# Performance work log

Hardware: AMD Instinct MI355X
Metric: run time of the kernel (lower is better)

The kernel has to match this reference:

```python
import jax, jax.numpy as jnp
import numpy as np

NH = 4
ATT = 16
COL = 64
AIS = 64
B = 8192
SK = 200


def setup_inputs() -> dict:
    key = jax.random.key(0)
    k1, k2, k3, k4, k5 = jax.random.split(key, 5)
    # Xavier-uniform bounds for [fan_in, fan_out] matrices
    def xavier(k, fan_in, fan_out):
        bound = float(np.sqrt(6.0 / (fan_in + fan_out)))
        return jax.random.uniform(k, (fan_in, fan_out), jnp.float32, -bound, bound)
    return {
        "query_input": jax.random.normal(k1, (B, 1, COL), jnp.float32),
        "action_list_input": jax.random.normal(k2, (B, SK, AIS), jnp.float32),
        "Q": xavier(k3, COL, ATT * NH),
        "K": xavier(k4, AIS, ATT * NH),
        "V": xavier(k5, AIS, ATT * NH),
    }


def reference(query_input, action_list_input, Q, K, V):
    b = query_input.shape[0]
    sq = query_input.shape[1]          # == 1 (required by final reshape)
    sk = action_list_input.shape[1]
    # projections
    q = jnp.tensordot(query_input, Q, axes=([-1], [0]))        # [B,Sq,NH*ATT]
    k = jnp.tensordot(action_list_input, K, axes=([-1], [0]))  # [B,Sk,NH*ATT]
    v = jnp.tensordot(action_list_input, V, axes=([-1], [0]))  # [B,Sk,NH*ATT]
    # split heads: chunk along last dim then stack on new leading dim -> [NH,B,S,ATT]
    qh = jnp.transpose(q.reshape(b, sq, NH, ATT), (2, 0, 1, 3))
    kh = jnp.transpose(k.reshape(b, sk, NH, ATT), (2, 0, 1, 3))
    vh = jnp.transpose(v.reshape(b, sk, NH, ATT), (2, 0, 1, 3))
    scores = jnp.einsum("hbqd,hbkd->hbqk", qh, kh) / 8.0       # [NH,B,Sq,Sk]
    attn = jax.nn.softmax(scores, axis=-1)
    res = jnp.einsum("hbqk,hbkd->hbqd", attn, vh)              # [NH,B,Sq,ATT]
    res = jnp.transpose(res, (1, 2, 0, 3))                     # [B,Sq,NH,ATT]
    return res.reshape(b, NH * ATT)
```

## Files before the change

kernel.cpp:

```cpp
#include <hip/hip_runtime.h>

#define NH  4
#define ATT 16
#define COL 64
#define AIS 64
#define SK  200
#define HD  (NH * ATT)
#define AST (AIS + 1)

__global__ __launch_bounds__(256)
void qk_precompute(const float* __restrict__ query,
                   const float* __restrict__ Qw,
                   const float* __restrict__ Kw,
                   float* __restrict__ qk) {
    __shared__ float qv_s[COL];
    __shared__ float qh_s[HD];
    const int b = blockIdx.x;
    const int t = threadIdx.x;

    if (t < COL) qv_s[t] = query[(size_t)b * COL + t];
    __syncthreads();

    if (t < HD) {
        float acc = 0.f;
        #pragma unroll
        for (int c = 0; c < COL; ++c)
            acc = fmaf(qv_s[c], Qw[c * HD + t], acc);
        qh_s[t] = acc;
    }
    __syncthreads();

    const int h = t >> 6;
    const int j = t & 63;
    float acc = 0.f;
    #pragma unroll
    for (int d = 0; d < ATT; ++d)
        acc = fmaf(qh_s[h * ATT + d], Kw[j * HD + h * ATT + d], acc);
    qk[(size_t)b * (NH * AIS) + t] = acc * 0.125f;
}

__global__ __launch_bounds__(256, 2)
void attn_main(const float* __restrict__ action,
               const float* __restrict__ Vw,
               const float* __restrict__ qk,
               float* __restrict__ out) {
    __shared__ float A[SK * AST];
    __shared__ float p_s[NH][SK];
    __shared__ float w_s[NH * AIS];
    __shared__ float invd_s[NH];

    const int b    = blockIdx.x;
    const int t    = threadIdx.x;
    const int lane = t & 63;
    const int wv   = t >> 6;

    const float4* act4 = (const float4*)(action + (size_t)b * (SK * AIS));
    #pragma unroll
    for (int i = 0; i < 13; ++i) {
        const int idx = i * 256 + t;
        if (idx < SK * AIS / 4) {
            const float4 v = act4[idx];
            const int e = idx << 2;
            const int k = e >> 6;
            const int j = e & 63;
            float* dst = &A[k * AST + j];
            dst[0] = v.x; dst[1] = v.y; dst[2] = v.z; dst[3] = v.w;
        }
    }
    __syncthreads();

    const float* qkb = qk + (size_t)b * (NH * AIS);
    if (t < SK) {
        float a0 = 0.f, a1 = 0.f, a2 = 0.f, a3 = 0.f;
        const int base = t * AST;
        #pragma unroll 8
        for (int j = 0; j < AIS; ++j) {
            const float a = A[base + j];
            a0 = fmaf(a, qkb[0 * AIS + j], a0);
            a1 = fmaf(a, qkb[1 * AIS + j], a1);
            a2 = fmaf(a, qkb[2 * AIS + j], a2);
            a3 = fmaf(a, qkb[3 * AIS + j], a3);
        }
        p_s[0][t] = a0; p_s[1][t] = a1; p_s[2][t] = a2; p_s[3][t] = a3;
    }
    __syncthreads();

    {
        const int h = wv;
        const float s0 = p_s[h][lane];
        const float s1 = p_s[h][lane + 64];
        const float s2 = p_s[h][lane + 128];
        const float s3 = (lane < SK - 192) ? p_s[h][192 + lane] : -1e30f;
        float m = fmaxf(fmaxf(s0, s1), fmaxf(s2, s3));
        #pragma unroll
        for (int off = 32; off; off >>= 1) m = fmaxf(m, __shfl_xor(m, off));
        const float e0 = __expf(s0 - m);
        const float e1 = __expf(s1 - m);
        const float e2 = __expf(s2 - m);
        const float e3 = (lane < SK - 192) ? __expf(s3 - m) : 0.f;
        p_s[h][lane]       = e0;
        p_s[h][lane + 64]  = e1;
        p_s[h][lane + 128] = e2;
        if (lane < SK - 192) p_s[h][192 + lane] = e3;
        float sum = e0 + e1 + e2 + e3;
        #pragma unroll
        for (int off = 32; off; off >>= 1) sum += __shfl_xor(sum, off);
        if (lane == 0) invd_s[h] = 1.f / sum;
    }
    __syncthreads();

    {
        const int h = wv, j = lane;
        float acc = 0.f;
        #pragma unroll 4
        for (int k = 0; k < SK; ++k)
            acc = fmaf(p_s[h][k], A[k * AST + j], acc);
        w_s[h * AIS + j] = acc;
    }
    __syncthreads();

    if (t < HD) {
        const int h = t >> 4;
        float acc = 0.f;
        #pragma unroll
        for (int j = 0; j < AIS; ++j)
            acc = fmaf(w_s[h * AIS + j], Vw[j * HD + t], acc);
        out[(size_t)b * HD + t] = acc * invd_s[h];
    }
}

extern "C" void kernel_launch(void* const* d_in, const int* in_sizes, int n_in,
                              void* d_out, int out_size, void* d_ws, size_t ws_size,
                              hipStream_t stream) {
    const float* query  = (const float*)d_in[0];
    const float* action = (const float*)d_in[1];
    const float* Qw     = (const float*)d_in[2];
    const float* Kw     = (const float*)d_in[3];
    const float* Vw     = (const float*)d_in[4];
    float* outp = (float*)d_out;

    const int B = in_sizes[0] / COL;
    float* qkbuf = (float*)d_ws;

    qk_precompute<<<B, 256, 0, stream>>>(query, Qw, Kw, qkbuf);
    attn_main<<<B, 256, 0, stream>>>(action, Vw, qkbuf, outp);
}
```

Baseline: 640.9 us.

## Store action tile as packed fp16 in LDS and use dot2 for scores

The action tile is stored in shared memory as packed half2, which halves LDS footprint and allows four blocks per CU. Scores are computed with fp16 dot2 against packed fp16 query-key vectors, and the weighted sum over keys is split across all four waves with a reduction. The qk precompute kernel now handles four batches per block. The fp16 conversion adds rounding error to both scores and values, which may affect accuracy tolerance.

```diff
diff --git a/kernel.cpp b/kernel.cpp
--- a/kernel.cpp
+++ b/kernel.cpp
@@ -1,53 +1,80 @@
 #include <hip/hip_runtime.h>
 
-#define NH  4
-#define ATT 16
-#define COL 64
-#define AIS 64
-#define SK  200
-#define HD  (NH * ATT)
-#define AST (AIS + 1)
+#define NH   4
+#define ATT  16
+#define COL  64
+#define AIS  64
+#define SK   200
+#define HD   64
+#define JP   32
+#define AROW 33
+
+typedef _Float16 half2v __attribute__((ext_vector_type(2)));
+typedef unsigned int uint32;
+
+static __device__ __forceinline__ half2v u2h(uint32 u) {
+    union { uint32 u; half2v h; } x; x.u = u; return x.h;
+}
+
+static __device__ __forceinline__ uint32 pk_u32(float a, float b) {
+#if __has_builtin(__builtin_amdgcn_cvt_pkrtz)
+    union { decltype(__builtin_amdgcn_cvt_pkrtz(0.f, 0.f)) h; uint32 u; } x;
+    x.h = __builtin_amdgcn_cvt_pkrtz(a, b);
+    return x.u;
+#else
+    union { half2v h; uint32 u; } x;
+    x.h.x = (_Float16)a; x.h.y = (_Float16)b;
+    return x.u;
+#endif
+}
+
+#if __has_builtin(__builtin_amdgcn_fdot2)
+#define DOT2(a, b, c) __builtin_amdgcn_fdot2((a), (b), (c), false)
+#else
+#define DOT2(a, b, c) fmaf((float)(a).x, (float)(b).x, fmaf((float)(a).y, (float)(b).y, (c)))
+#endif
 
 __global__ __launch_bounds__(256)
-void qk_precompute(const float* __restrict__ query,
-                   const float* __restrict__ Qw,
-                   const float* __restrict__ Kw,
-                   float* __restrict__ qk) {
-    __shared__ float qv_s[COL];
+void qk_kernel(const float* __restrict__ query, const float* __restrict__ Qw,
+               const float* __restrict__ Kw, uint32* __restrict__ qk2, int nb) {
     __shared__ float qh_s[HD];
-    const int b = blockIdx.x;
     const int t = threadIdx.x;
-
-    if (t < COL) qv_s[t] = query[(size_t)b * COL + t];
-    __syncthreads();
-
-    if (t < HD) {
-        float acc = 0.f;
-        #pragma unroll
-        for (int c = 0; c < COL; ++c)
-            acc = fmaf(qv_s[c], Qw[c * HD + t], acc);
-        qh_s[t] = acc;
+    #pragma unroll
+    for (int bb = 0; bb < 4; ++bb) {
+        const int b = blockIdx.x * 4 + bb;
+        if (b >= nb) break;
+        const float* qb = query + (size_t)b * COL;
+        if (t < HD) {
+            float acc = 0.f;
+            #pragma unroll
+            for (int c = 0; c < COL; ++c)
+                acc = fmaf(qb[c], Qw[c * HD + t], acc);
+            qh_s[t] = acc;
+        }
+        __syncthreads();
+        if (t < 128) {
+            const int h = t >> 5, jp = t & 31;
+            float a0 = 0.f, a1 = 0.f;
+            #pragma unroll
+            for (int d = 0; d < ATT; ++d) {
+                const float q = qh_s[h * ATT + d];
+                a0 = fmaf(q, Kw[(2 * jp)     * HD + h * ATT + d], a0);
+                a1 = fmaf(q, Kw[(2 * jp + 1) * HD + h * ATT + d], a1);
+            }
+            qk2[(size_t)b * 128 + t] = pk_u32(a0 * 0.125f, a1 * 0.125f);
+        }
+        __syncthreads();
     }
-    __syncthreads();
-
-    const int h = t >> 6;
-    const int j = t & 63;
-    float acc = 0.f;
-    #pragma unroll
-    for (int d = 0; d < ATT; ++d)
-        acc = fmaf(qh_s[h * ATT + d], Kw[j * HD + h * ATT + d], acc);
-    qk[(size_t)b * (NH * AIS) + t] = acc * 0.125f;
 }
 
-__global__ __launch_bounds__(256, 2)
-void attn_main(const float* __restrict__ action,
-               const float* __restrict__ Vw,
-               const float* __restrict__ qk,
-               float* __restrict__ out) {
-    __shared__ float A[SK * AST];
-    __shared__ float p_s[NH][SK];
-    __shared__ float w_s[NH * AIS];
-    __shared__ float invd_s[NH];
+__global__ __launch_bounds__(256, 4)
+void attn_kernel(const float* __restrict__ action, const float* __restrict__ Vw,
+                 const uint32* __restrict__ qk2, float* __restrict__ out) {
+    __shared__ uint32 A2[SK * AROW];
+    __shared__ float4 p4_s[SK];
+    __shared__ float4 wpart[4][64];
+    __shared__ float4 w4_s[64];
+    __shared__ float  invd_s[NH];
 
     const int b    = blockIdx.x;
     const int t    = threadIdx.x;
@@ -60,37 +87,38 @@
         const int idx = i * 256 + t;
         if (idx < SK * AIS / 4) {
             const float4 v = act4[idx];
-            const int e = idx << 2;
-            const int k = e >> 6;
-            const int j = e & 63;
-            float* dst = &A[k * AST + j];
-            dst[0] = v.x; dst[1] = v.y; dst[2] = v.z; dst[3] = v.w;
+            const int k   = idx >> 4;
+            const int jp0 = (idx & 15) * 2;
+            A2[k * AROW + jp0]     = pk_u32(v.x, v.y);
+            A2[k * AROW + jp0 + 1] = pk_u32(v.z, v.w);
         }
     }
     __syncthreads();
 
-    const float* qkb = qk + (size_t)b * (NH * AIS);
+    const uint32* qkb = qk2 + (size_t)b * 128;
     if (t < SK) {
         float a0 = 0.f, a1 = 0.f, a2 = 0.f, a3 = 0.f;
-        const int base = t * AST;
+        const int base = t * AROW;
         #pragma unroll 8
-        for (int j = 0; j < AIS; ++j) {
-            const float a = A[base + j];
-            a0 = fmaf(a, qkb[0 * AIS + j], a0);
-            a1 = fmaf(a, qkb[1 * AIS + j], a1);
-            a2 = fmaf(a, qkb[2 * AIS + j], a2);
-            a3 = fmaf(a, qkb[3 * AIS + j], a3);
+        for (int jp = 0; jp < JP; ++jp) {
+            const half2v av = u2h(A2[base + jp]);
+            a0 = DOT2(av, u2h(qkb[jp]),      a0);
+            a1 = DOT2(av, u2h(qkb[32 + jp]), a1);
+            a2 = DOT2(av, u2h(qkb[64 + jp]), a2);
+            a3 = DOT2(av, u2h(qkb[96 + jp]), a3);
         }
-        p_s[0][t] = a0; p_s[1][t] = a1; p_s[2][t] = a2; p_s[3][t] = a3;
+        float4 s; s.x = a0; s.y = a1; s.z = a2; s.w = a3;
+        p4_s[t] = s;
     }
     __syncthreads();
 
     {
+        float* pf = (float*)p4_s;
         const int h = wv;
-        const float s0 = p_s[h][lane];
-        const float s1 = p_s[h][lane + 64];
-        const float s2 = p_s[h][lane + 128];
-        const float s3 = (lane < SK - 192) ? p_s[h][192 + lane] : -1e30f;
+        const float s0 = pf[lane * 4 + h];
+        const float s1 = pf[(lane + 64) * 4 + h];
+        const float s2 = pf[(lane + 128) * 4 + h];
+        const float s3 = (lane < SK - 192) ? pf[(lane + 192) * 4 + h] : -1e30f;
         float m = fmaxf(fmaxf(s0, s1), fmaxf(s2, s3));
         #pragma unroll
         for (int off = 32; off; off >>= 1) m = fmaxf(m, __shfl_xor(m, off));
@@ -98,10 +126,10 @@
         const float e1 = __expf(s1 - m);
         const float e2 = __expf(s2 - m);
         const float e3 = (lane < SK - 192) ? __expf(s3 - m) : 0.f;
-        p_s[h][lane]       = e0;
-        p_s[h][lane + 64]  = e1;
-        p_s[h][lane + 128] = e2;
-        if (lane < SK - 192) p_s[h][192 + lane] = e3;
+        pf[lane * 4 + h]         = e0;
+        pf[(lane + 64) * 4 + h]  = e1;
+        pf[(lane + 128) * 4 + h] = e2;
+        if (lane < SK - 192) pf[(lane + 192) * 4 + h] = e3;
         float sum = e0 + e1 + e2 + e3;
         #pragma unroll
         for (int off = 32; off; off >>= 1) sum += __shfl_xor(sum, off);
@@ -110,22 +138,46 @@
     __syncthreads();
 
     {
-        const int h = wv, j = lane;
-        float acc = 0.f;
-        #pragma unroll 4
-        for (int k = 0; k < SK; ++k)
-            acc = fmaf(p_s[h][k], A[k * AST + j], acc);
-        w_s[h * AIS + j] = acc;
+        const int j  = lane;
+        const int jp = j >> 1;
+        const int k0 = wv * 50;
+        float c0 = 0.f, c1 = 0.f, c2 = 0.f, c3 = 0.f;
+        #pragma unroll 10
+        for (int kk = 0; kk < 50; ++kk) {
+            const int k = k0 + kk;
+            const float4 p = p4_s[k];
+            const half2v av = u2h(A2[k * AROW + jp]);
+            const float a = (j & 1) ? (float)av.y : (float)av.x;
+            c0 = fmaf(p.x, a, c0);
+            c1 = fmaf(p.y, a, c1);
+            c2 = fmaf(p.z, a, c2);
+            c3 = fmaf(p.w, a, c3);
+        }
+        float4 c; c.x = c0; c.y = c1; c.z = c2; c.w = c3;
+        wpart[wv][j] = c;
     }
     __syncthreads();
 
-    if (t < HD) {
+    if (t < 64) {
+        const float4 r0 = wpart[0][t], r1 = wpart[1][t];
+        const float4 r2 = wpart[2][t], r3 = wpart[3][t];
+        float4 w;
+        w.x = (r0.x + r1.x + r2.x + r3.x) * invd_s[0];
+        w.y = (r0.y + r1.y + r2.y + r3.y) * invd_s[1];
+        w.z = (r0.z + r1.z + r2.z + r3.z) * invd_s[2];
+        w.w = (r0.w + r1.w + r2.w + r3.w) * invd_s[3];
+        w4_s[t] = w;
+    }
+    __syncthreads();
+
+    if (t < 64) {
         const int h = t >> 4;
+        const float* wf = (const float*)w4_s;
         float acc = 0.f;
         #pragma unroll
         for (int j = 0; j < AIS; ++j)
-            acc = fmaf(w_s[h * AIS + j], Vw[j * HD + t], acc);
-        out[(size_t)b * HD + t] = acc * invd_s[h];
+            acc = fmaf(wf[j * 4 + h], Vw[j * HD + t], acc);
+        out[(size_t)b * HD + t] = acc;
     }
 }
 
@@ -140,8 +192,8 @@
     float* outp = (float*)d_out;
 
     const int B = in_sizes[0] / COL;
-    float* qkbuf = (float*)d_ws;
+    uint32* qk2 = (uint32*)d_ws;
 
-    qk_precompute<<<B, 256, 0, stream>>>(query, Qw, Kw, qkbuf);
-    attn_main<<<B, 256, 0, stream>>>(action, Vw, qkbuf, outp);
+    qk_kernel<<<(B + 3) / 4, 256, 0, stream>>>(query, Qw, Kw, qk2, B);
+    attn_kernel<<<B, 256, 0, stream>>>(action, Vw, qk2, outp);
 }
```

Measured after the change: 581.3 us. -9.3%, faster.
